# Performance work log

Hardware: AMD Instinct MI355X
Metric: run time of the kernel (lower is better)

The kernel has to match this reference:

```python
import jax, jax.numpy as jnp
import numpy as np

HEAD_DIM = 128
N_HEADS = 32
N_KV_HEADS = 8
N_REP = N_HEADS // N_KV_HEADS


def _rope(t, cos, sin):
    # t: [b, s, h, d]; cos/sin: [s, d//2]; rotate interleaved pairs (complex mult)
    b, s, h, d = t.shape
    t = t.reshape(b, s, h, d // 2, 2)
    t0, t1 = t[..., 0], t[..., 1]
    c = cos[None, :, None, :]
    sn = sin[None, :, None, :]
    r0 = t0 * c - t1 * sn
    r1 = t0 * sn + t1 * c
    return jnp.stack([r0, r1], axis=-1).reshape(b, s, h, d)


def setup_inputs() -> dict:
    key = jax.random.key(0)
    ks = jax.random.split(key, 6)
    b, s, dim = 2, 2048, 4096
    x = jax.random.normal(ks[0], (b, s, dim), dtype=jnp.float32)
    wq = jax.random.normal(ks[1], (N_HEADS * HEAD_DIM, dim), dtype=jnp.float32) * 0.02
    wk = jax.random.normal(ks[2], (N_KV_HEADS * HEAD_DIM, dim), dtype=jnp.float32) * 0.02
    wv = jax.random.normal(ks[3], (N_KV_HEADS * HEAD_DIM, dim), dtype=jnp.float32) * 0.02
    wo = jax.random.normal(ks[4], (dim, N_HEADS * HEAD_DIM), dtype=jnp.float32) * 0.02
    # precompute_freqs_cis: theta = 10000, freqs over half head_dim
    inv = 1.0 / (10000.0 ** (np.arange(0, HEAD_DIM, 2)[: HEAD_DIM // 2] / HEAD_DIM))
    ang = np.outer(np.arange(s), inv).astype(np.float32)  # [s, d//2]
    freqs_cos = jnp.asarray(np.cos(ang))
    freqs_sin = jnp.asarray(np.sin(ang))
    # causal additive mask
    mask = jnp.triu(jnp.full((s, s), -jnp.inf, dtype=jnp.float32), k=1)
    return {"x": x, "wq": wq, "wk": wk, "wv": wv, "wo": wo,
            "freqs_cos": freqs_cos, "freqs_sin": freqs_sin, "mask": mask,
            "start_pos": 0}


def reference(x, wq, wk, wv, wo, freqs_cos, freqs_sin, mask, start_pos):
    b, s, dim = x.shape
    xq = (x @ wq.T).reshape(b, s, N_HEADS, HEAD_DIM)
    xk = (x @ wk.T).reshape(b, s, N_KV_HEADS, HEAD_DIM)
    xv = (x @ wv.T).reshape(b, s, N_KV_HEADS, HEAD_DIM)
    xq = _rope(xq, freqs_cos, freqs_sin)
    xk = _rope(xk, freqs_cos, freqs_sin)
    # full prefill (start_pos=0): keys/values == current xk/xv
    # GQA via broadcast instead of materialized repeat_kv (same math)
    q = xq.transpose(0, 2, 1, 3).reshape(b, N_KV_HEADS, N_REP, s, HEAD_DIM)
    k = xk.transpose(0, 2, 1, 3)  # [b, kvh, s, d]
    v = xv.transpose(0, 2, 1, 3)
    scores = jnp.einsum('bgnqd,bgkd->bgnqk', q, k) / jnp.sqrt(
        jnp.asarray(HEAD_DIM, dtype=x.dtype))
    scores = scores + mask[None, None, None, :, :]
    probs = jax.nn.softmax(scores.astype(jnp.float32), axis=-1).astype(x.dtype)
    out = jnp.einsum('bgnqk,bgkd->bgnqd', probs, v)  # [b, kvh, n_rep, s, d]
    out = out.reshape(b, N_HEADS, s, HEAD_DIM).transpose(0, 2, 1, 3).reshape(b, s, -1)
    return out @ wo.T
```

## Files before the change

kernel.cpp:

```cpp
#include <hip/hip_runtime.h>
#include <hip/hip_fp16.h>
#include <stdint.h>
#include <stddef.h>

typedef _Float16 f16;
typedef __attribute__((ext_vector_type(4))) _Float16 f16x4;
typedef __attribute__((ext_vector_type(8))) _Float16 f16x8;
typedef __attribute__((ext_vector_type(4))) float f32x4;
typedef __attribute__((ext_vector_type(16))) float f32x16;

__device__ __forceinline__ void gld_lds16(const void* g, void* l) {
  __builtin_amdgcn_global_load_lds((const __attribute__((address_space(1))) void*)g,
                                   (__attribute__((address_space(3))) void*)l, 16, 0, 0);
}

__global__ void cast_all(const float* __restrict__ x, const float* __restrict__ wq,
                         const float* __restrict__ wk, const float* __restrict__ wv,
                         const float* __restrict__ wo, f16* __restrict__ xh,
                         f16* __restrict__ wqh, f16* __restrict__ wkh,
                         f16* __restrict__ wvh, f16* __restrict__ woh) {
  int i = blockIdx.x * blockDim.x + threadIdx.x;
  const float* in;
  f16* out;
  int j = i;
  if (j < 4194304) { in = x; out = xh; }
  else if ((j -= 4194304) < 4194304) { in = wq; out = wqh; }
  else if ((j -= 4194304) < 1048576) { in = wk; out = wkh; }
  else if ((j -= 1048576) < 1048576) { in = wv; out = wvh; }
  else { j -= 1048576; in = wo; out = woh; }
  float4 v = ((const float4*)in)[j];
  f16x4 h;
  h[0] = (f16)v.x; h[1] = (f16)v.y; h[2] = (f16)v.z; h[3] = (f16)v.w;
  *(f16x4*)(out + (size_t)j * 4) = h;
}

__device__ __forceinline__ void gemm_core_4096(const f16* __restrict__ Ab,
                                               const f16* __restrict__ Bb,
                                               f16* As, f16* Bs, f32x16 acc[2][2]) {
  const int tid = threadIdx.x, ln = tid & 63, wv = tid >> 6;
  const int wr = wv >> 1, wc = wv & 1;
  const int l31 = ln & 31, half = ln >> 5;
#pragma unroll
  for (int a = 0; a < 2; ++a)
#pragma unroll
    for (int b = 0; b < 2; ++b)
#pragma unroll
      for (int r = 0; r < 16; ++r) acc[a][b][r] = 0.f;

  int srow[2], scol[2];
#pragma unroll
  for (int c = 0; c < 2; ++c) {
    int chunk = wv * 2 + c;
    int lineL = chunk * 8 + (ln >> 3);
    int s = (ln & 7) ^ (lineL & 7);
    srow[c] = lineL * 2 + (s >> 2);
    scol[c] = (s & 3) * 8;
  }
  const int rb = l31 >> 1;
  const int bxor = ((l31 & 1) * 4) ^ (rb & 7);

  for (int k0 = 0; k0 < 4096; k0 += 32) {
#pragma unroll
    for (int c = 0; c < 2; ++c) {
      int chunk = wv * 2 + c;
      gld_lds16(Ab + (size_t)srow[c] * 4096 + k0 + scol[c], As + chunk * 512);
      gld_lds16(Bb + (size_t)srow[c] * 4096 + k0 + scol[c], Bs + chunk * 512);
    }
    __syncthreads();
    f16x8 af[2][2], bf[2][2];
#pragma unroll
    for (int tm = 0; tm < 2; ++tm) {
      int lbase = (wr * 32 + tm * 16 + rb) * 64;
#pragma unroll
      for (int ks = 0; ks < 2; ++ks)
        af[tm][ks] = *(const f16x8*)&As[lbase + (((ks * 2 + half) ^ bxor) * 8)];
    }
#pragma unroll
    for (int tn = 0; tn < 2; ++tn) {
      int lbase = (wc * 32 + tn * 16 + rb) * 64;
#pragma unroll
      for (int ks = 0; ks < 2; ++ks)
        bf[tn][ks] = *(const f16x8*)&Bs[lbase + (((ks * 2 + half) ^ bxor) * 8)];
    }
#pragma unroll
    for (int tm = 0; tm < 2; ++tm)
#pragma unroll
      for (int tn = 0; tn < 2; ++tn) {
        acc[tm][tn] = __builtin_amdgcn_mfma_f32_32x32x16_f16(af[tm][0], bf[tn][0], acc[tm][tn], 0, 0, 0);
        acc[tm][tn] = __builtin_amdgcn_mfma_f32_32x32x16_f16(af[tm][1], bf[tn][1], acc[tm][tn], 0, 0, 0);
      }
    __syncthreads();
  }
}

__global__ __launch_bounds__(256, 4) void gemm_qkv(
    const f16* __restrict__ xh, const f16* __restrict__ wqh,
    const f16* __restrict__ wkh, const f16* __restrict__ wvh,
    f16* __restrict__ qh, f16* __restrict__ kh, f16* __restrict__ vt) {
  __shared__ __align__(16) f16 As[4096];
  __shared__ __align__(16) f16 Bs[4096];
  const int bx = blockIdx.x, by = blockIdx.y;
  const f16* Bb;
  if (bx < 32)      Bb = wqh + (size_t)bx * 128 * 4096;
  else if (bx < 40) Bb = wkh + (size_t)(bx - 32) * 128 * 4096;
  else              Bb = wvh + (size_t)(bx - 40) * 128 * 4096;
  f32x16 acc[2][2];
  gemm_core_4096(xh + (size_t)by * 128 * 4096, Bb, As, Bs, acc);
  const int tid = threadIdx.x, ln = tid & 63, wv = tid >> 6;
  const int wr = wv >> 1, wc = wv & 1;
  const int l31 = ln & 31, half = ln >> 5;
#pragma unroll
  for (int tm = 0; tm < 2; ++tm)
#pragma unroll
    for (int tn = 0; tn < 2; ++tn) {
      int colb = wc * 64 + tn * 32 + l31;
#pragma unroll
      for (int g = 0; g < 4; ++g) {
        int mb = by * 128 + wr * 64 + tm * 32 + g * 8 + half * 4;
        if (bx < 32) {
#pragma unroll
          for (int r2 = 0; r2 < 4; ++r2)
            qh[(size_t)(mb + r2) * 4096 + bx * 128 + colb] = (f16)acc[tm][tn][g * 4 + r2];
        } else if (bx < 40) {
#pragma unroll
          for (int r2 = 0; r2 < 4; ++r2)
            kh[(size_t)(mb + r2) * 1024 + (bx - 32) * 128 + colb] = (f16)acc[tm][tn][g * 4 + r2];
        } else {
          f16x4 v4;
#pragma unroll
          for (int r2 = 0; r2 < 4; ++r2) v4[r2] = (f16)acc[tm][tn][g * 4 + r2];
          int n2 = (bx - 40) * 128 + colb;
          int kv = n2 >> 7, d = n2 & 127;
          int bbv = mb >> 11, sl = mb & 2047;
          *(f16x4*)&vt[(((size_t)bbv * 8 + kv) * 128 + d) * 2048 + sl] = v4;
        }
      }
    }
}

__global__ void rope_qk(f16* __restrict__ qh, f16* __restrict__ kh,
                        const float* __restrict__ fc, const float* __restrict__ fs) {
  int i = blockIdx.x * blockDim.x + threadIdx.x;
  const int QG = 4096 * 32 * 16;
  f16* ptr;
  int sl, p0;
  if (i < QG) {
    int g = i & 15, head = (i >> 4) & 31, tok = i >> 9;
    sl = tok & 2047; p0 = g * 4;
    ptr = qh + (size_t)tok * 4096 + head * 128 + g * 8;
  } else {
    int j = i - QG;
    int g = j & 15, head = (j >> 4) & 7, tok = j >> 7;
    sl = tok & 2047; p0 = g * 4;
    ptr = kh + (size_t)tok * 1024 + head * 128 + g * 8;
  }
  f16x8 v = *(f16x8*)ptr;
  float4 c = *(const float4*)&fc[sl * 64 + p0];
  float4 s = *(const float4*)&fs[sl * 64 + p0];
  f16x8 o;
  o[0] = (f16)((float)v[0] * c.x - (float)v[1] * s.x);
  o[1] = (f16)((float)v[0] * s.x + (float)v[1] * c.x);
  o[2] = (f16)((float)v[2] * c.y - (float)v[3] * s.y);
  o[3] = (f16)((float)v[2] * s.y + (float)v[3] * c.y);
  o[4] = (f16)((float)v[4] * c.z - (float)v[5] * s.z);
  o[5] = (f16)((float)v[4] * s.z + (float)v[5] * c.z);
  o[6] = (f16)((float)v[6] * c.w - (float)v[7] * s.w);
  o[7] = (f16)((float)v[6] * s.w + (float)v[7] * c.w);
  *(f16x8*)ptr = o;
}

__global__ __launch_bounds__(256, 4) void attn(
    const f16* __restrict__ qh, const f16* __restrict__ kh,
    const f16* __restrict__ vt, f16* __restrict__ ao) {
  __shared__ __align__(16) f16 Kl[64 * 128];
  __shared__ __align__(16) f16 Vl[128 * 64];
  __shared__ __align__(16) f16 Pl[4][16 * 64];
  const int qt = 31 - blockIdx.x;
  const int h = blockIdx.y, bb = blockIdx.z;
  const int kvh = h >> 2;
  const int tid = threadIdx.x, ln = tid & 63, wv = tid >> 6;
  const int quad = ln >> 4, c16 = ln & 15;

  f16x8 Qf[4];
  {
    size_t qbase = ((size_t)(bb * 2048 + qt * 64 + wv * 16 + c16)) * 4096 + h * 128;
#pragma unroll
    for (int ks = 0; ks < 4; ++ks)
      Qf[ks] = *(const f16x8*)&qh[qbase + ks * 32 + quad * 8];
  }
  float m_run = -INFINITY, l_run = 0.f;
  f32x4 Ot[8];
#pragma unroll
  for (int n = 0; n < 8; ++n) { f32x4 z = {0.f, 0.f, 0.f, 0.f}; Ot[n] = z; }
  const float scale = 0.08838834764831843f;
  const int qg = qt * 64 + wv * 16 + c16;
  const int swp = ((quad ^ (c16 & 7)) * 8);
  const int swp1 = (((4 + quad) ^ (c16 & 7)) * 8);

  for (int t = 0; t <= qt; ++t) {
#pragma unroll
    for (int c = 0; c < 4; ++c) {
      int chunk = wv * 4 + c;
      int krow = chunk * 4 + (ln >> 4);
      int kg = (ln & 15) ^ (krow & 15);
      gld_lds16(&kh[((size_t)(bb * 2048 + t * 64 + krow)) * 1024 + kvh * 128 + kg * 8],
                &Kl[chunk * 512]);
    }
#pragma unroll
    for (int c = 0; c < 4; ++c) {
      int chunk = wv * 4 + c;
      int vrow = chunk * 8 + (ln >> 3);
      int vg = (ln & 7) ^ (vrow & 7);
      gld_lds16(&vt[(((size_t)bb * 8 + kvh) * 128 + vrow) * 2048 + t * 64 + vg * 8],
                &Vl[chunk * 512]);
    }
    __syncthreads();

    f32x4 Sa[4];
#pragma unroll
    for (int tn = 0; tn < 4; ++tn) {
      f32x4 z = {0.f, 0.f, 0.f, 0.f};
      Sa[tn] = z;
#pragma unroll
      for (int ks = 0; ks < 4; ++ks) {
        f16x8 kf = *(const f16x8*)&Kl[(tn * 16 + c16) * 128 + (((ks * 4 + quad) ^ c16) * 8)];
        Sa[tn] = __builtin_amdgcn_mfma_f32_16x16x32_f16(kf, Qf[ks], Sa[tn], 0, 0, 0);
      }
    }

#pragma unroll
    for (int tn = 0; tn < 4; ++tn)
#pragma unroll
      for (int r = 0; r < 4; ++r) Sa[tn][r] *= scale;
    if (t == qt) {
#pragma unroll
      for (int tn = 0; tn < 4; ++tn) {
        int kbase = t * 64 + tn * 16 + quad * 4;
#pragma unroll
        for (int r = 0; r < 4; ++r)
          if (kbase + r > qg) Sa[tn][r] = -INFINITY;
      }
    }

    float mm = -INFINITY;
#pragma unroll
    for (int tn = 0; tn < 4; ++tn)
#pragma unroll
      for (int r = 0; r < 4; ++r) mm = fmaxf(mm, Sa[tn][r]);
    mm = fmaxf(mm, __shfl_xor(mm, 16, 64));
    mm = fmaxf(mm, __shfl_xor(mm, 32, 64));
    float mn = fmaxf(m_run, mm);
    float alpha = __expf(m_run - mn);
    m_run = mn;
    float rsum = 0.f;
#pragma unroll
    for (int tn = 0; tn < 4; ++tn)
#pragma unroll
      for (int r = 0; r < 4; ++r) {
        float p = __expf(Sa[tn][r] - mn);
        Sa[tn][r] = p;
        rsum += p;
      }
    rsum += __shfl_xor(rsum, 16, 64);
    rsum += __shfl_xor(rsum, 32, 64);
    l_run = l_run * alpha + rsum;

#pragma unroll
    for (int tn = 0; tn < 4; ++tn) {
      f16x4 pk;
#pragma unroll
      for (int r = 0; r < 4; ++r) pk[r] = (f16)Sa[tn][r];
      int g = tn * 2 + (quad >> 1);
      *(f16x4*)&Pl[wv][c16 * 64 + ((g ^ (c16 & 7)) * 8) + (quad & 1) * 4] = pk;
    }

#pragma unroll
    for (int n = 0; n < 8; ++n)
#pragma unroll
      for (int r = 0; r < 4; ++r) Ot[n][r] *= alpha;

    __asm__ volatile("s_waitcnt lgkmcnt(0)" ::: "memory");

    {
      f16x8 pf0 = *(const f16x8*)&Pl[wv][c16 * 64 + swp];
      f16x8 pf1 = *(const f16x8*)&Pl[wv][c16 * 64 + swp1];
#pragma unroll
      for (int n = 0; n < 8; ++n) {
        int rowv = (n * 16 + c16) * 64;
        f16x8 vf0 = *(const f16x8*)&Vl[rowv + swp];
        Ot[n] = __builtin_amdgcn_mfma_f32_16x16x32_f16(vf0, pf0, Ot[n], 0, 0, 0);
        f16x8 vf1 = *(const f16x8*)&Vl[rowv + swp1];
        Ot[n] = __builtin_amdgcn_mfma_f32_16x16x32_f16(vf1, pf1, Ot[n], 0, 0, 0);
      }
    }
    __syncthreads();
  }

  float inv = 1.0f / l_run;
  size_t token = (size_t)(bb * 2048 + qt * 64 + wv * 16 + c16);
#pragma unroll
  for (int n = 0; n < 8; ++n) {
    f16x4 o;
#pragma unroll
    for (int r = 0; r < 4; ++r) o[r] = (f16)(Ot[n][r] * inv);
    *(f16x4*)&ao[token * 4096 + h * 128 + n * 16 + quad * 4] = o;
  }
}

__global__ __launch_bounds__(256, 4) void gemm_out(
    const f16* __restrict__ ao, const f16* __restrict__ woh, float* __restrict__ out) {
  __shared__ __align__(16) f16 As[4096];
  __shared__ __align__(16) f16 Bs[4096];
  f32x16 acc[2][2];
  gemm_core_4096(ao + (size_t)blockIdx.y * 128 * 4096,
                 woh + (size_t)blockIdx.x * 128 * 4096, As, Bs, acc);
  const int tid = threadIdx.x, ln = tid & 63, wv = tid >> 6;
  const int wr = wv >> 1, wc = wv & 1;
  const int l31 = ln & 31, half = ln >> 5;
#pragma unroll
  for (int tm = 0; tm < 2; ++tm)
#pragma unroll
    for (int tn = 0; tn < 2; ++tn) {
      int n = blockIdx.x * 128 + wc * 64 + tn * 32 + l31;
#pragma unroll
      for (int g = 0; g < 4; ++g) {
        int mb = blockIdx.y * 128 + wr * 64 + tm * 32 + g * 8 + half * 4;
#pragma unroll
        for (int r2 = 0; r2 < 4; ++r2)
          out[(size_t)(mb + r2) * 4096 + n] = acc[tm][tn][g * 4 + r2];
      }
    }
}

extern "C" void kernel_launch(void* const* d_in, const int* in_sizes, int n_in,
                              void* d_out, int out_size, void* d_ws, size_t ws_size,
                              hipStream_t stream) {
  const float* x  = (const float*)d_in[0];
  const float* wq = (const float*)d_in[1];
  const float* wk = (const float*)d_in[2];
  const float* wv = (const float*)d_in[3];
  const float* wo = (const float*)d_in[4];
  const float* fc = (const float*)d_in[5];
  const float* fs = (const float*)d_in[6];
  float* out = (float*)d_out;

  char* ws = (char*)d_ws;
  f16* xh  = (f16*)(ws + 0);
  f16* wqh = (f16*)(ws + 33554432);
  f16* wkh = (f16*)(ws + 67108864);
  f16* wvh = (f16*)(ws + 75497472);
  f16* woh = (f16*)(ws + 83886080);
  f16* qh  = (f16*)(ws + 117440512);
  f16* kh  = (f16*)(ws + 150994944);
  f16* vt  = (f16*)(ws + 159383552);
  f16* ao  = (f16*)(ws + 167772160);

  cast_all<<<57344, 256, 0, stream>>>(x, wq, wk, wv, wo, xh, wqh, wkh, wvh, woh);
  gemm_qkv<<<dim3(48, 32), 256, 0, stream>>>(xh, wqh, wkh, wvh, qh, kh, vt);
  rope_qk<<<10240, 256, 0, stream>>>(qh, kh, fc, fs);
  attn<<<dim3(32, 32, 2), 256, 0, stream>>>(qh, kh, vt, ao);
  gemm_out<<<dim3(32, 32), 256, 0, stream>>>(ao, woh, out);
}
```

Baseline: 870.7 us.

## Enlarge GEMM M-tile to 256 and attention Q-tile to 128 rows per block

The shared GEMM core now computes a 256x128 tile per block, with each wave holding a 4x2 grid of 32x32 accumulators. This doubles B-tile reuse and halves the grids of the QKV and output projections. The attention kernel now processes 128 query rows per block, two 16-row subtiles per wave, so each K/V tile loaded into LDS is reused for twice as many queries. In exchange, register and LDS use grow (launch bounds drop to 2 blocks per SM), fewer blocks are launched, and the causal load imbalance per block gets coarser.

```diff
diff --git a/kernel.cpp b/kernel.cpp
--- a/kernel.cpp
+++ b/kernel.cpp
@@ -36,41 +36,49 @@
 
 __device__ __forceinline__ void gemm_core_4096(const f16* __restrict__ Ab,
                                                const f16* __restrict__ Bb,
-                                               f16* As, f16* Bs, f32x16 acc[2][2]) {
+                                               f16* As, f16* Bs, f32x16 acc[4][2]) {
   const int tid = threadIdx.x, ln = tid & 63, wv = tid >> 6;
   const int wr = wv >> 1, wc = wv & 1;
   const int l31 = ln & 31, half = ln >> 5;
 #pragma unroll
-  for (int a = 0; a < 2; ++a)
+  for (int a = 0; a < 4; ++a)
 #pragma unroll
     for (int b = 0; b < 2; ++b)
 #pragma unroll
       for (int r = 0; r < 16; ++r) acc[a][b][r] = 0.f;
 
-  int srow[2], scol[2];
+  int srA[4], scA[4], srB[2], scB[2];
+#pragma unroll
+  for (int c = 0; c < 4; ++c) {
+    int chunk = wv * 4 + c;
+    int lineL = chunk * 8 + (ln >> 3);
+    int s = (ln & 7) ^ (lineL & 7);
+    srA[c] = lineL * 2 + (s >> 2);
+    scA[c] = (s & 3) * 8;
+  }
 #pragma unroll
   for (int c = 0; c < 2; ++c) {
     int chunk = wv * 2 + c;
     int lineL = chunk * 8 + (ln >> 3);
     int s = (ln & 7) ^ (lineL & 7);
-    srow[c] = lineL * 2 + (s >> 2);
-    scol[c] = (s & 3) * 8;
+    srB[c] = lineL * 2 + (s >> 2);
+    scB[c] = (s & 3) * 8;
   }
   const int rb = l31 >> 1;
   const int bxor = ((l31 & 1) * 4) ^ (rb & 7);
 
   for (int k0 = 0; k0 < 4096; k0 += 32) {
 #pragma unroll
-    for (int c = 0; c < 2; ++c) {
-      int chunk = wv * 2 + c;
-      gld_lds16(Ab + (size_t)srow[c] * 4096 + k0 + scol[c], As + chunk * 512);
-      gld_lds16(Bb + (size_t)srow[c] * 4096 + k0 + scol[c], Bs + chunk * 512);
-    }
+    for (int c = 0; c < 4; ++c)
+      gld_lds16(Ab + (size_t)srA[c] * 4096 + k0 + scA[c], As + (wv * 4 + c) * 512);
+#pragma unroll
+    for (int c = 0; c < 2; ++c)
+      gld_lds16(Bb + (size_t)srB[c] * 4096 + k0 + scB[c], Bs + (wv * 2 + c) * 512);
     __syncthreads();
-    f16x8 af[2][2], bf[2][2];
-#pragma unroll
-    for (int tm = 0; tm < 2; ++tm) {
-      int lbase = (wr * 32 + tm * 16 + rb) * 64;
+    f16x8 af[4][2], bf[2][2];
+#pragma unroll
+    for (int tm = 0; tm < 4; ++tm) {
+      int lbase = (wr * 64 + tm * 16 + rb) * 64;
 #pragma unroll
       for (int ks = 0; ks < 2; ++ks)
         af[tm][ks] = *(const f16x8*)&As[lbase + (((ks * 2 + half) ^ bxor) * 8)];
@@ -83,7 +91,7 @@
         bf[tn][ks] = *(const f16x8*)&Bs[lbase + (((ks * 2 + half) ^ bxor) * 8)];
     }
 #pragma unroll
-    for (int tm = 0; tm < 2; ++tm)
+    for (int tm = 0; tm < 4; ++tm)
 #pragma unroll
       for (int tn = 0; tn < 2; ++tn) {
         acc[tm][tn] = __builtin_amdgcn_mfma_f32_32x32x16_f16(af[tm][0], bf[tn][0], acc[tm][tn], 0, 0, 0);
@@ -93,30 +101,30 @@
   }
 }
 
-__global__ __launch_bounds__(256, 4) void gemm_qkv(
+__global__ __launch_bounds__(256, 2) void gemm_qkv(
     const f16* __restrict__ xh, const f16* __restrict__ wqh,
     const f16* __restrict__ wkh, const f16* __restrict__ wvh,
     f16* __restrict__ qh, f16* __restrict__ kh, f16* __restrict__ vt) {
-  __shared__ __align__(16) f16 As[4096];
+  __shared__ __align__(16) f16 As[8192];
   __shared__ __align__(16) f16 Bs[4096];
   const int bx = blockIdx.x, by = blockIdx.y;
   const f16* Bb;
   if (bx < 32)      Bb = wqh + (size_t)bx * 128 * 4096;
   else if (bx < 40) Bb = wkh + (size_t)(bx - 32) * 128 * 4096;
   else              Bb = wvh + (size_t)(bx - 40) * 128 * 4096;
-  f32x16 acc[2][2];
-  gemm_core_4096(xh + (size_t)by * 128 * 4096, Bb, As, Bs, acc);
+  f32x16 acc[4][2];
+  gemm_core_4096(xh + (size_t)by * 256 * 4096, Bb, As, Bs, acc);
   const int tid = threadIdx.x, ln = tid & 63, wv = tid >> 6;
   const int wr = wv >> 1, wc = wv & 1;
   const int l31 = ln & 31, half = ln >> 5;
 #pragma unroll
-  for (int tm = 0; tm < 2; ++tm)
+  for (int tm = 0; tm < 4; ++tm)
 #pragma unroll
     for (int tn = 0; tn < 2; ++tn) {
       int colb = wc * 64 + tn * 32 + l31;
 #pragma unroll
       for (int g = 0; g < 4; ++g) {
-        int mb = by * 128 + wr * 64 + tm * 32 + g * 8 + half * 4;
+        int mb = by * 256 + wr * 128 + tm * 32 + g * 8 + half * 4;
         if (bx < 32) {
 #pragma unroll
           for (int r2 = 0; r2 < 4; ++r2)
@@ -169,35 +177,41 @@
   *(f16x8*)ptr = o;
 }
 
-__global__ __launch_bounds__(256, 4) void attn(
+__global__ __launch_bounds__(256, 2) void attn(
     const f16* __restrict__ qh, const f16* __restrict__ kh,
     const f16* __restrict__ vt, f16* __restrict__ ao) {
   __shared__ __align__(16) f16 Kl[64 * 128];
   __shared__ __align__(16) f16 Vl[128 * 64];
-  __shared__ __align__(16) f16 Pl[4][16 * 64];
-  const int qt = 31 - blockIdx.x;
+  __shared__ __align__(16) f16 Pl[4][32 * 64];
+  const int qb = 15 - blockIdx.x;
   const int h = blockIdx.y, bb = blockIdx.z;
   const int kvh = h >> 2;
   const int tid = threadIdx.x, ln = tid & 63, wv = tid >> 6;
   const int quad = ln >> 4, c16 = ln & 15;
 
-  f16x8 Qf[4];
-  {
-    size_t qbase = ((size_t)(bb * 2048 + qt * 64 + wv * 16 + c16)) * 4096 + h * 128;
+  f16x8 Qf[2][4];
+#pragma unroll
+  for (int st = 0; st < 2; ++st) {
+    size_t qbase = ((size_t)(bb * 2048 + qb * 128 + wv * 32 + st * 16 + c16)) * 4096 + h * 128;
 #pragma unroll
     for (int ks = 0; ks < 4; ++ks)
-      Qf[ks] = *(const f16x8*)&qh[qbase + ks * 32 + quad * 8];
-  }
-  float m_run = -INFINITY, l_run = 0.f;
-  f32x4 Ot[8];
-#pragma unroll
-  for (int n = 0; n < 8; ++n) { f32x4 z = {0.f, 0.f, 0.f, 0.f}; Ot[n] = z; }
+      Qf[st][ks] = *(const f16x8*)&qh[qbase + ks * 32 + quad * 8];
+  }
+  float m_run[2] = {-INFINITY, -INFINITY}, l_run[2] = {0.f, 0.f};
+  f32x4 Ot[2][8];
+#pragma unroll
+  for (int st = 0; st < 2; ++st)
+#pragma unroll
+    for (int n = 0; n < 8; ++n) { f32x4 z = {0.f, 0.f, 0.f, 0.f}; Ot[st][n] = z; }
   const float scale = 0.08838834764831843f;
-  const int qg = qt * 64 + wv * 16 + c16;
-  const int swp = ((quad ^ (c16 & 7)) * 8);
-  const int swp1 = (((4 + quad) ^ (c16 & 7)) * 8);
-
-  for (int t = 0; t <= qt; ++t) {
+  int qg[2];
+  qg[0] = qb * 128 + wv * 32 + c16;
+  qg[1] = qg[0] + 16;
+  const int swk0 = ((quad ^ (c16 & 7)) * 8);
+  const int swk1 = (((4 + quad) ^ (c16 & 7)) * 8);
+  const int nt = 2 * qb + 2;
+
+  for (int t = 0; t < nt; ++t) {
 #pragma unroll
     for (int c = 0; c < 4; ++c) {
       int chunk = wv * 4 + c;
@@ -216,115 +230,126 @@
     }
     __syncthreads();
 
-    f32x4 Sa[4];
+    f32x4 Sa[2][4];
 #pragma unroll
     for (int tn = 0; tn < 4; ++tn) {
       f32x4 z = {0.f, 0.f, 0.f, 0.f};
-      Sa[tn] = z;
+      Sa[0][tn] = z; Sa[1][tn] = z;
 #pragma unroll
       for (int ks = 0; ks < 4; ++ks) {
         f16x8 kf = *(const f16x8*)&Kl[(tn * 16 + c16) * 128 + (((ks * 4 + quad) ^ c16) * 8)];
-        Sa[tn] = __builtin_amdgcn_mfma_f32_16x16x32_f16(kf, Qf[ks], Sa[tn], 0, 0, 0);
-      }
-    }
-
-#pragma unroll
-    for (int tn = 0; tn < 4; ++tn)
-#pragma unroll
-      for (int r = 0; r < 4; ++r) Sa[tn][r] *= scale;
-    if (t == qt) {
+        Sa[0][tn] = __builtin_amdgcn_mfma_f32_16x16x32_f16(kf, Qf[0][ks], Sa[0][tn], 0, 0, 0);
+        Sa[1][tn] = __builtin_amdgcn_mfma_f32_16x16x32_f16(kf, Qf[1][ks], Sa[1][tn], 0, 0, 0);
+      }
+    }
+
+#pragma unroll
+    for (int st = 0; st < 2; ++st)
+#pragma unroll
+      for (int tn = 0; tn < 4; ++tn)
+#pragma unroll
+        for (int r = 0; r < 4; ++r) Sa[st][tn][r] *= scale;
+    if (t >= 2 * qb) {
+#pragma unroll
+      for (int st = 0; st < 2; ++st)
+#pragma unroll
+        for (int tn = 0; tn < 4; ++tn) {
+          int kbase = t * 64 + tn * 16 + quad * 4;
+#pragma unroll
+          for (int r = 0; r < 4; ++r)
+            if (kbase + r > qg[st]) Sa[st][tn][r] = -INFINITY;
+        }
+    }
+
+#pragma unroll
+    for (int st = 0; st < 2; ++st) {
+      float mm = -INFINITY;
+#pragma unroll
+      for (int tn = 0; tn < 4; ++tn)
+#pragma unroll
+        for (int r = 0; r < 4; ++r) mm = fmaxf(mm, Sa[st][tn][r]);
+      mm = fmaxf(mm, __shfl_xor(mm, 16, 64));
+      mm = fmaxf(mm, __shfl_xor(mm, 32, 64));
+      float mn = fmaxf(m_run[st], mm);
+      float alpha = __expf(m_run[st] - mn);
+      m_run[st] = mn;
+      float rsum = 0.f;
+#pragma unroll
+      for (int tn = 0; tn < 4; ++tn)
+#pragma unroll
+        for (int r = 0; r < 4; ++r) {
+          float p = __expf(Sa[st][tn][r] - mn);
+          Sa[st][tn][r] = p;
+          rsum += p;
+        }
+      rsum += __shfl_xor(rsum, 16, 64);
+      rsum += __shfl_xor(rsum, 32, 64);
+      l_run[st] = l_run[st] * alpha + rsum;
+
 #pragma unroll
       for (int tn = 0; tn < 4; ++tn) {
-        int kbase = t * 64 + tn * 16 + quad * 4;
-#pragma unroll
-        for (int r = 0; r < 4; ++r)
-          if (kbase + r > qg) Sa[tn][r] = -INFINITY;
-      }
-    }
-
-    float mm = -INFINITY;
-#pragma unroll
-    for (int tn = 0; tn < 4; ++tn)
-#pragma unroll
-      for (int r = 0; r < 4; ++r) mm = fmaxf(mm, Sa[tn][r]);
-    mm = fmaxf(mm, __shfl_xor(mm, 16, 64));
-    mm = fmaxf(mm, __shfl_xor(mm, 32, 64));
-    float mn = fmaxf(m_run, mm);
-    float alpha = __expf(m_run - mn);
-    m_run = mn;
-    float rsum = 0.f;
-#pragma unroll
-    for (int tn = 0; tn < 4; ++tn)
-#pragma unroll
-      for (int r = 0; r < 4; ++r) {
-        float p = __expf(Sa[tn][r] - mn);
-        Sa[tn][r] = p;
-        rsum += p;
-      }
-    rsum += __shfl_xor(rsum, 16, 64);
-    rsum += __shfl_xor(rsum, 32, 64);
-    l_run = l_run * alpha + rsum;
-
-#pragma unroll
-    for (int tn = 0; tn < 4; ++tn) {
-      f16x4 pk;
-#pragma unroll
-      for (int r = 0; r < 4; ++r) pk[r] = (f16)Sa[tn][r];
-      int g = tn * 2 + (quad >> 1);
-      *(f16x4*)&Pl[wv][c16 * 64 + ((g ^ (c16 & 7)) * 8) + (quad & 1) * 4] = pk;
-    }
-
-#pragma unroll
-    for (int n = 0; n < 8; ++n)
-#pragma unroll
-      for (int r = 0; r < 4; ++r) Ot[n][r] *= alpha;
+        f16x4 pk;
+#pragma unroll
+        for (int r = 0; r < 4; ++r) pk[r] = (f16)Sa[st][tn][r];
+        int g = tn * 2 + (quad >> 1);
+        *(f16x4*)&Pl[wv][(st * 16 + c16) * 64 + ((g ^ (c16 & 7)) * 8) + (quad & 1) * 4] = pk;
+      }
+
+#pragma unroll
+      for (int n = 0; n < 8; ++n)
+#pragma unroll
+        for (int r = 0; r < 4; ++r) Ot[st][n][r] *= alpha;
+    }
 
     __asm__ volatile("s_waitcnt lgkmcnt(0)" ::: "memory");
 
-    {
-      f16x8 pf0 = *(const f16x8*)&Pl[wv][c16 * 64 + swp];
-      f16x8 pf1 = *(const f16x8*)&Pl[wv][c16 * 64 + swp1];
+#pragma unroll
+    for (int ks = 0; ks < 2; ++ks) {
+      int sw = ks ? swk1 : swk0;
+      f16x8 pf0 = *(const f16x8*)&Pl[wv][c16 * 64 + sw];
+      f16x8 pf1 = *(const f16x8*)&Pl[wv][(16 + c16) * 64 + sw];
 #pragma unroll
       for (int n = 0; n < 8; ++n) {
-        int rowv = (n * 16 + c16) * 64;
-        f16x8 vf0 = *(const f16x8*)&Vl[rowv + swp];
-        Ot[n] = __builtin_amdgcn_mfma_f32_16x16x32_f16(vf0, pf0, Ot[n], 0, 0, 0);
-        f16x8 vf1 = *(const f16x8*)&Vl[rowv + swp1];
-        Ot[n] = __builtin_amdgcn_mfma_f32_16x16x32_f16(vf1, pf1, Ot[n], 0, 0, 0);
+        f16x8 vf = *(const f16x8*)&Vl[(n * 16 + c16) * 64 + sw];
+        Ot[0][n] = __builtin_amdgcn_mfma_f32_16x16x32_f16(vf, pf0, Ot[0][n], 0, 0, 0);
+        Ot[1][n] = __builtin_amdgcn_mfma_f32_16x16x32_f16(vf, pf1, Ot[1][n], 0, 0, 0);
       }
     }
     __syncthreads();
   }
 
-  float inv = 1.0f / l_run;
-  size_t token = (size_t)(bb * 2048 + qt * 64 + wv * 16 + c16);
-#pragma unroll
-  for (int n = 0; n < 8; ++n) {
-    f16x4 o;
-#pragma unroll
-    for (int r = 0; r < 4; ++r) o[r] = (f16)(Ot[n][r] * inv);
-    *(f16x4*)&ao[token * 4096 + h * 128 + n * 16 + quad * 4] = o;
-  }
-}
-
-__global__ __launch_bounds__(256, 4) void gemm_out(
+#pragma unroll
+  for (int st = 0; st < 2; ++st) {
+    float inv = 1.0f / l_run[st];
+    size_t token = (size_t)(bb * 2048 + qb * 128 + wv * 32 + st * 16 + c16);
+#pragma unroll
+    for (int n = 0; n < 8; ++n) {
+      f16x4 o;
+#pragma unroll
+      for (int r = 0; r < 4; ++r) o[r] = (f16)(Ot[st][n][r] * inv);
+      *(f16x4*)&ao[token * 4096 + h * 128 + n * 16 + quad * 4] = o;
+    }
+  }
+}
+
+__global__ __launch_bounds__(256, 2) void gemm_out(
     const f16* __restrict__ ao, const f16* __restrict__ woh, float* __restrict__ out) {
-  __shared__ __align__(16) f16 As[4096];
+  __shared__ __align__(16) f16 As[8192];
   __shared__ __align__(16) f16 Bs[4096];
-  f32x16 acc[2][2];
-  gemm_core_4096(ao + (size_t)blockIdx.y * 128 * 4096,
+  f32x16 acc[4][2];
+  gemm_core_4096(ao + (size_t)blockIdx.y * 256 * 4096,
                  woh + (size_t)blockIdx.x * 128 * 4096, As, Bs, acc);
   const int tid = threadIdx.x, ln = tid & 63, wv = tid >> 6;
   const int wr = wv >> 1, wc = wv & 1;
   const int l31 = ln & 31, half = ln >> 5;
 #pragma unroll
-  for (int tm = 0; tm < 2; ++tm)
+  for (int tm = 0; tm < 4; ++tm)
 #pragma unroll
     for (int tn = 0; tn < 2; ++tn) {
       int n = blockIdx.x * 128 + wc * 64 + tn * 32 + l31;
 #pragma unroll
       for (int g = 0; g < 4; ++g) {
-        int mb = blockIdx.y * 128 + wr * 64 + tm * 32 + g * 8 + half * 4;
+        int mb = blockIdx.y * 256 + wr * 128 + tm * 32 + g * 8 + half * 4;
 #pragma unroll
         for (int r2 = 0; r2 < 4; ++r2)
           out[(size_t)(mb + r2) * 4096 + n] = acc[tm][tn][g * 4 + r2];
@@ -356,8 +381,8 @@
   f16* ao  = (f16*)(ws + 167772160);
 
   cast_all<<<57344, 256, 0, stream>>>(x, wq, wk, wv, wo, xh, wqh, wkh, wvh, woh);
-  gemm_qkv<<<dim3(48, 32), 256, 0, stream>>>(xh, wqh, wkh, wvh, qh, kh, vt);
+  gemm_qkv<<<dim3(48, 16), 256, 0, stream>>>(xh, wqh, wkh, wvh, qh, kh, vt);
   rope_qk<<<10240, 256, 0, stream>>>(qh, kh, fc, fs);
-  attn<<<dim3(32, 32, 2), 256, 0, stream>>>(qh, kh, vt, ao);
-  gemm_out<<<dim3(32, 32), 256, 0, stream>>>(ao, woh, out);
-}
+  attn<<<dim3(16, 32, 2), 256, 0, stream>>>(qh, kh, vt, ao);
+  gemm_out<<<dim3(32, 16), 256, 0, stream>>>(ao, woh, out);
+}
```

Result: no change. 882.7 us (+1.4%).
